# Kernel tuning notes

Hardware: AMD Instinct MI355X
Metric: run time of the kernel (lower is better)

Reference implementation:

```python
import jax, jax.numpy as jnp
import numpy as np
from jax import lax

B, P, ENC = 64, 196, 2048
E, H, A, V = 512, 512, 512, 10000
L = 21  # caption length -> T = 20 decode steps


def setup_inputs() -> dict:
    key = jax.random.key(0)
    ks = jax.random.split(key, 20)
    s = 0.02
    inp = {
        "features": jax.random.normal(ks[0], (B, P, ENC), jnp.float32),
        "captions": jax.random.randint(ks[1], (B, L), 0, V),
        # attention
        "W_enc_att": jax.random.normal(ks[2], (ENC, A), jnp.float32) * s,
        "b_enc_att": jnp.zeros((A,), jnp.float32),
        "W_dec_att": jax.random.normal(ks[3], (H, A), jnp.float32) * s,
        "b_dec_att": jnp.zeros((A,), jnp.float32),
        "W_full": jax.random.normal(ks[4], (A, 1), jnp.float32) * s,
        "b_full": jnp.zeros((1,), jnp.float32),
        # embedding (uniform(-0.1, 0.1) as in init_weights)
        "emb": jax.random.uniform(ks[5], (V, E), jnp.float32, -0.1, 0.1),
        # LSTMCell: input = embed + encoder_dim, gate order i,f,g,o
        "W_ih": jax.random.normal(ks[6], (E + ENC, 4 * H), jnp.float32) * s,
        "W_hh": jax.random.normal(ks[7], (H, 4 * H), jnp.float32) * s,
        "b_ih": jnp.zeros((4 * H,), jnp.float32),
        "b_hh": jnp.zeros((4 * H,), jnp.float32),
        # init state projections
        "W_init_h": jax.random.normal(ks[8], (ENC, H), jnp.float32) * s,
        "b_init_h": jnp.zeros((H,), jnp.float32),
        "W_init_c": jax.random.normal(ks[9], (ENC, H), jnp.float32) * s,
        "b_init_c": jnp.zeros((H,), jnp.float32),
        # gating
        "W_fbeta": jax.random.normal(ks[10], (H, ENC), jnp.float32) * s,
        "b_fbeta": jnp.zeros((ENC,), jnp.float32),
        # output fc (uniform(-0.1,0.1), bias 0)
        "W_fc": jax.random.uniform(ks[11], (H, V), jnp.float32, -0.1, 0.1),
        "b_fc": jnp.zeros((V,), jnp.float32),
    }
    return inp


def reference(features, captions, W_enc_att, b_enc_att, W_dec_att, b_dec_att,
              W_full, b_full, emb, W_ih, W_hh, b_ih, b_hh,
              W_init_h, b_init_h, W_init_c, b_init_c,
              W_fbeta, b_fbeta, W_fc, b_fc):
    # init hidden state from mean-pooled encoder features
    mean_enc = features.mean(axis=1)                       # [B, ENC]
    h0 = mean_enc @ W_init_h + b_init_h                    # [B, H]
    c0 = mean_enc @ W_init_c + b_init_c

    # encoder-side attention projection is time-invariant: precompute
    att1 = features @ W_enc_att + b_enc_att                # [B, P, A]

    T = captions.shape[1] - 1                              # decode_lengths = L-1 (equal lengths)
    embs = emb[captions[:, :T]]                            # [B, T, E]
    embs_t = jnp.swapaxes(embs, 0, 1)                      # [T, B, E]

    def step(carry, e_t):
        h, c = carry
        att2 = h @ W_dec_att + b_dec_att                   # [B, A]
        scores = (jax.nn.relu(att1 + att2[:, None, :]) @ W_full)[..., 0] + b_full  # [B, P]
        alpha = jax.nn.softmax(scores, axis=1)
        awe = jnp.einsum('bp,bpe->be', alpha, features)    # [B, ENC]
        gate = jax.nn.sigmoid(h @ W_fbeta + b_fbeta)
        awe = gate * awe
        x = jnp.concatenate([e_t, awe], axis=1)            # [B, E+ENC]
        gates = x @ W_ih + h @ W_hh + b_ih + b_hh          # [B, 4H]
        i, f, g, o = jnp.split(gates, 4, axis=1)
        c_new = jax.nn.sigmoid(f) * c + jax.nn.sigmoid(i) * jnp.tanh(g)
        h_new = jax.nn.sigmoid(o) * jnp.tanh(c_new)
        preds = h_new @ W_fc + b_fc                        # dropout in eval mode = identity
        return (h_new, c_new), preds

    _, preds = lax.scan(step, (h0, c0), embs_t)            # [T, B, V]
    return jnp.swapaxes(preds, 0, 1)                       # [B, T, V]
```

## Files before the change

### kernel.cpp

```cpp
#include <hip/hip_runtime.h>
#include <hip/hip_bf16.h>


#define TB 256

typedef __bf16 bf16x8 __attribute__((ext_vector_type(8)));
typedef float f32x4 __attribute__((ext_vector_type(4)));
typedef unsigned short u16x8 __attribute__((ext_vector_type(8)));
typedef unsigned short u16x4 __attribute__((ext_vector_type(4)));
typedef unsigned short ushort_t;

__device__ __forceinline__ ushort_t f2bf(float x) {
    unsigned u = __builtin_bit_cast(unsigned, x);
    u += 0x7fffu + ((u >> 16) & 1u);
    return (ushort_t)(u >> 16);
}
__device__ __forceinline__ float bf2f(ushort_t b) {
    return __builtin_bit_cast(float, (unsigned)b << 16);
}
__device__ __forceinline__ void store_pack(
    ushort_t* __restrict__ Ph, ushort_t* __restrict__ Pl,
    int KC, int m, int k, float v)
{
    const size_t flat = ((((size_t)(m >> 4) * KC + (k >> 5)) * 64)
                         + ((k & 31) >> 3) * 16 + (m & 15)) * 8 + (k & 7);
    const ushort_t h = f2bf(v);
    Ph[flat] = h;
    Pl[flat] = f2bf(v - bf2f(h));
}

struct PackJobs {
    const float* W[7];
    ushort_t* Bh[7];
    ushort_t* Bl[7];
    int Nsrc[7], ntCount[7], KC[7], ntBase[7];
    int cum[8];
};

__global__ __launch_bounds__(TB) void pack_all(PackJobs J)
{
    const int blk = blockIdx.x;
    int j = 0;
    #pragma unroll
    for (int i = 1; i < 7; ++i) if (blk >= J.cum[i]) j = i;
    const int g = (blk - J.cum[j]) * TB + threadIdx.x;
    const int KC = J.KC[j];
    const int lane = g & 63;
    const int kc = (g >> 6) % KC;
    const int nt = g / (64 * KC);
    if (nt >= J.ntCount[j]) return;
    const int Nsrc = J.Nsrc[j];
    const float* W = J.W[j];
    const int n = nt * 16 + (lane & 15);
    const int kb = kc * 32 + (lane >> 4) * 8;
    u16x8 hv, lv;
    #pragma unroll
    for (int e = 0; e < 8; ++e) {
        const float x = (n < Nsrc) ? W[(size_t)(kb + e) * Nsrc + n] : 0.f;
        const ushort_t h = f2bf(x);
        hv[e] = h;
        lv[e] = f2bf(x - bf2f(h));
    }
    const size_t flat = (((size_t)(J.ntBase[j] + nt) * KC + kc) * 64 + lane) * 8;
    *(u16x8*)&J.Bh[j][flat] = hv;
    *(u16x8*)&J.Bl[j][flat] = lv;
}

template<int MT, int NT, int WR, int WC>
__device__ __forceinline__ void mfma_tile(
    const ushort_t* lds, int wr, int wc, int lane,
    f32x4 acc[MT / WR][NT / WC])
{
    constexpr int MFR = MT / WR, NFR = NT / WC;
    bf16x8 ah[MFR], al[MFR];
    #pragma unroll
    for (int i = 0; i < MFR; ++i) {
        ah[i] = __builtin_bit_cast(bf16x8, *(const u16x8*)&lds[(wr * MFR + i) * 512 + lane * 8]);
        al[i] = __builtin_bit_cast(bf16x8, *(const u16x8*)&lds[(MT + wr * MFR + i) * 512 + lane * 8]);
    }
    #pragma unroll
    for (int j = 0; j < NFR; ++j) {
        const bf16x8 bh = __builtin_bit_cast(bf16x8, *(const u16x8*)&lds[(2 * MT + wc * NFR + j) * 512 + lane * 8]);
        const bf16x8 bl = __builtin_bit_cast(bf16x8, *(const u16x8*)&lds[(2 * MT + NT + wc * NFR + j) * 512 + lane * 8]);
        #pragma unroll
        for (int i = 0; i < MFR; ++i) {
            acc[i][j] = __builtin_amdgcn_mfma_f32_16x16x32_bf16(ah[i], bh, acc[i][j], 0, 0, 0);
            acc[i][j] = __builtin_amdgcn_mfma_f32_16x16x32_bf16(ah[i], bl, acc[i][j], 0, 0, 0);
            acc[i][j] = __builtin_amdgcn_mfma_f32_16x16x32_bf16(al[i], bh, acc[i][j], 0, 0, 0);
        }
    }
}

template<int MT, int NT, int WR, int WC>
__global__ __launch_bounds__(TB) void gemm_mfma(
    const ushort_t* __restrict__ Ah, const ushort_t* __restrict__ Al,
    const ushort_t* __restrict__ Bh, const ushort_t* __restrict__ Bl,
    int KC, int kcPer,
    const float* __restrict__ bias,
    float* __restrict__ C, int ldc, int Ncols, size_t cPartStride)
{
    constexpr int MFR = MT / WR, NFR = NT / WC, CH = 2 * (MT + NT);
    __shared__ __align__(16) ushort_t lds[CH * 512];
    const int tid = threadIdx.x, wid = tid >> 6, lane = tid & 63;
    const int wr = wid / WC, wc = wid % WC;

    const int tot = gridDim.x * gridDim.y;
    const int lin = blockIdx.x + gridDim.x * blockIdx.y;
    const int q = tot >> 3, r = tot & 7;
    const int xcd = lin & 7, jj = lin >> 3;
    const int base = (xcd < r) ? xcd * (q + 1) : r * (q + 1) + (xcd - r) * q;
    const int lin2 = base + jj;
    const int nb = lin2 / gridDim.y;
    const int mb = lin2 % gridDim.y;

    const int kc0 = blockIdx.z * kcPer;

    f32x4 acc[MFR][NFR];
    #pragma unroll
    for (int i = 0; i < MFR; ++i)
        #pragma unroll
        for (int j = 0; j < NFR; ++j)
            acc[i][j] = f32x4{0.f, 0.f, 0.f, 0.f};

    for (int kc = kc0; kc < kc0 + kcPer; ++kc) {
        __syncthreads();
        #pragma unroll
        for (int cc = 0; cc < CH / 4; ++cc) {
            const int c = cc * 4 + wid;
            const ushort_t* src;
            if (c < MT)                src = Ah + ((size_t)(mb * MT + c) * KC + kc) * 512;
            else if (c < 2 * MT)       src = Al + ((size_t)(mb * MT + c - MT) * KC + kc) * 512;
            else if (c < 2 * MT + NT)  src = Bh + ((size_t)(nb * NT + c - 2 * MT) * KC + kc) * 512;
            else                       src = Bl + ((size_t)(nb * NT + c - 2 * MT - NT) * KC + kc) * 512;
            *(u16x8*)&lds[c * 512 + lane * 8] = *(const u16x8*)(src + lane * 8);
        }
        __syncthreads();
        mfma_tile<MT, NT, WR, WC>(lds, wr, wc, lane, acc);
    }

    C += (size_t)blockIdx.z * cPartStride;
    #pragma unroll
    for (int i = 0; i < MFR; ++i)
        #pragma unroll
        for (int j = 0; j < NFR; ++j) {
            const int col = nb * NT * 16 + (wc * NFR + j) * 16 + (lane & 15);
            if (col < Ncols) {
                const float bv = bias ? bias[col] : 0.f;
                const int rbase = mb * MT * 16 + (wr * MFR + i) * 16 + ((lane >> 4) << 2);
                #pragma unroll
                for (int r2 = 0; r2 < 4; ++r2)
                    C[(size_t)(rbase + r2) * ldc + col] = acc[i][j][r2] + bv;
            }
        }
}

__global__ __launch_bounds__(TB) void gemm_att1(
    const float* __restrict__ A,
    const ushort_t* __restrict__ Bh, const ushort_t* __restrict__ Bl,
    const float* __restrict__ bias, float* __restrict__ C)
{
    __shared__ __align__(16) ushort_t lds[24 * 512];
    const int tid = threadIdx.x, wid = tid >> 6, lane = tid & 63;
    const int wr = wid >> 1, wc = wid & 1;

    const int lin = blockIdx.x + (blockIdx.y << 2);
    const int lin2 = (lin & 7) * 98 + (lin >> 3);
    const int nb = lin2 & 3, mb = lin2 >> 2;

    f32x4 acc[2][4];
    #pragma unroll
    for (int i = 0; i < 2; ++i)
        #pragma unroll
        for (int j = 0; j < 4; ++j)
            acc[i][j] = f32x4{0.f, 0.f, 0.f, 0.f};

    for (int kc = 0; kc < 64; ++kc) {
        __syncthreads();
        #pragma unroll
        for (int cc = 0; cc < 4; ++cc) {
            const int c = cc * 4 + wid;
            const ushort_t* src = (c < 8)
                ? Bh + ((size_t)(nb * 8 + c) * 64 + kc) * 512
                : Bl + ((size_t)(nb * 8 + c - 8) * 64 + kc) * 512;
            *(u16x8*)&lds[(8 + c) * 512 + lane * 8] = *(const u16x8*)(src + lane * 8);
        }
        #pragma unroll
        for (int p = 0; p < 2; ++p) {
            const int id = p * 256 + tid;
            const int row = id >> 3, c4 = id & 7;
            const float4 a = *(const float4*)&A[(size_t)(mb * 64 + row) * 2048 + kc * 32 + c4 * 4];
            const float xv[4] = {a.x, a.y, a.z, a.w};
            u16x4 hv, lv;
            #pragma unroll
            for (int qq = 0; qq < 4; ++qq) {
                const ushort_t h = f2bf(xv[qq]);
                hv[qq] = h;
                lv[qq] = f2bf(xv[qq] - bf2f(h));
            }
            const int base = ((c4 >> 1) * 16 + (row & 15)) * 8 + (c4 & 1) * 4;
            const int chunk = row >> 4;
            *(u16x4*)&lds[chunk * 512 + base] = hv;
            *(u16x4*)&lds[(4 + chunk) * 512 + base] = lv;
        }
        __syncthreads();
        mfma_tile<4, 8, 2, 2>(lds, wr, wc, lane, acc);
    }

    #pragma unroll
    for (int i = 0; i < 2; ++i)
        #pragma unroll
        for (int j = 0; j < 4; ++j) {
            const int col = nb * 128 + (wc * 4 + j) * 16 + (lane & 15);
            const float bv = bias[col];
            const int rbase = mb * 64 + (wr * 2 + i) * 16 + ((lane >> 4) << 2);
            #pragma unroll
            for (int r = 0; r < 4; ++r)
                C[(size_t)(rbase + r) * 512 + col] = acc[i][j][r] + bv;
        }
}

__device__ __forceinline__ void gemm_body(
    float (*As)[68], float (*Ws)[68],
    const float* __restrict__ A, int lda,
    const float* __restrict__ W, int ldw,
    float* __restrict__ C, int ldc,
    int nTile, int N, int K)
{
    const int tid = threadIdx.x;
    const int tn = tid & 15;
    const int tm = tid >> 4;
    const int n0 = nTile * 64;

    float acc[4][4] = {{0.f}};

    for (int k0 = 0; k0 < K; k0 += 32) {
        {
            int r  = tid >> 3;
            int cc = (tid & 7) * 4;
            #pragma unroll
            for (int rr = 0; rr < 64; rr += 32) {
                const float4 a = *(const float4*)&A[(size_t)(rr + r) * lda + (k0 + cc)];
                As[cc + 0][rr + r] = a.x;
                As[cc + 1][rr + r] = a.y;
                As[cc + 2][rr + r] = a.z;
                As[cc + 3][rr + r] = a.w;
            }
        }
        {
            int r  = tid >> 4;
            int cc = (tid & 15) * 4;
            #pragma unroll
            for (int rr = 0; rr < 32; rr += 16) {
                const float4 w = *(const float4*)&W[(size_t)(k0 + rr + r) * ldw + (n0 + cc)];
                *(float4*)&Ws[rr + r][cc] = w;
            }
        }
        __syncthreads();
        #pragma unroll
        for (int kk = 0; kk < 32; ++kk) {
            const float4 a = *(const float4*)&As[kk][tm * 4];
            const float4 w = *(const float4*)&Ws[kk][tn * 4];
            const float av[4] = {a.x, a.y, a.z, a.w};
            const float wv[4] = {w.x, w.y, w.z, w.w};
            #pragma unroll
            for (int i = 0; i < 4; ++i)
                #pragma unroll
                for (int j = 0; j < 4; ++j)
                    acc[i][j] = fmaf(av[i], wv[j], acc[i][j]);
        }
        __syncthreads();
    }

    #pragma unroll
    for (int i = 0; i < 4; ++i) {
        const int m = tm * 4 + i;
        #pragma unroll
        for (int j = 0; j < 4; ++j)
            C[(size_t)m * ldc + (n0 + tn * 4 + j)] = acc[i][j];
    }
}

__global__ __launch_bounds__(TB) void gemm_hc(
    const float* __restrict__ mean,
    const float* __restrict__ Wh0, const float* __restrict__ Wc0,
    float* __restrict__ h0p, float* __restrict__ c0p)
{
    __shared__ float As[32][68];
    __shared__ float Ws[32][68];
    const int ks = blockIdx.y & 7;
    const int which = blockIdx.y >> 3;
    const float* W = which ? Wc0 : Wh0;
    float* Cp = which ? c0p : h0p;
    gemm_body(As, Ws,
              mean + (size_t)ks * 256, 2048,
              W + (size_t)ks * 256 * 512, 512,
              Cp + (size_t)ks * 64 * 512, 512,
              blockIdx.x, 512, 256);
}

__global__ __launch_bounds__(TB) void scores_k(
    const float* __restrict__ att1,
    const float* __restrict__ hga_part,
    const float* __restrict__ bd,
    const float* __restrict__ Wfull,
    float* __restrict__ scores)
{
    const int b = blockIdx.x;
    const int tid = threadIdx.x;
    const int wave = tid >> 6;
    const int lane = tid & 63;

    __shared__ float a2[512];
    __shared__ float wf[512];

    for (int i = tid; i < 512; i += TB) {
        float v = bd[i];
        #pragma unroll
        for (int s = 0; s < 4; ++s)
            v += hga_part[(size_t)s * 64 * 4608 + (size_t)b * 4608 + i];
        a2[i] = v;
        wf[i] = Wfull[i];
    }
    __syncthreads();

    const int p = blockIdx.y * 4 + wave;
    const float* row = att1 + ((size_t)b * 196 + p) * 512;
    float s = 0.f;
    #pragma unroll
    for (int c = 0; c < 512; c += 256) {
        const int k = c + lane * 4;
        const float4 v = *(const float4*)&row[k];
        const float4 av = *(const float4*)&a2[k];
        const float4 wv = *(const float4*)&wf[k];
        s = fmaf(fmaxf(v.x + av.x, 0.f), wv.x, s);
        s = fmaf(fmaxf(v.y + av.y, 0.f), wv.y, s);
        s = fmaf(fmaxf(v.z + av.z, 0.f), wv.z, s);
        s = fmaf(fmaxf(v.w + av.w, 0.f), wv.w, s);
    }
    #pragma unroll
    for (int o = 32; o; o >>= 1) s += __shfl_xor(s, o);
    if (lane == 0) scores[b * 196 + p] = s;
}

__global__ __launch_bounds__(TB) void awe_gate(
    const float* __restrict__ scores,
    const float* __restrict__ features,
    const float* __restrict__ hga_part,
    const float* __restrict__ bf,
    ushort_t* __restrict__ gPh, ushort_t* __restrict__ gPl)
{
    const int b = blockIdx.y, chunk = blockIdx.x;
    const int tid = threadIdx.x;
    const int q = tid >> 6, lane = tid & 63;

    __shared__ float al[196];
    __shared__ float redm[4], reds[4];
    __shared__ float smq[4][256];

    const float sv = (tid < 196) ? scores[b * 196 + tid] : -1e30f;
    float m = sv;
    #pragma unroll
    for (int o = 32; o; o >>= 1) m = fmaxf(m, __shfl_xor(m, o));
    if (lane == 0) redm[q] = m;
    __syncthreads();
    m = fmaxf(fmaxf(redm[0], redm[1]), fmaxf(redm[2], redm[3]));

    const float e = (tid < 196) ? expf(sv - m) : 0.f;
    float s = e;
    #pragma unroll
    for (int o = 32; o; o >>= 1) s += __shfl_xor(s, o);
    if (lane == 0) reds[q] = s;
    __syncthreads();
    s = reds[0] + reds[1] + reds[2] + reds[3];

    if (tid < 196) al[tid] = e / s;
    __syncthreads();

    const int col0 = chunk * 256 + lane * 4;
    const float* f = features + (size_t)b * 196 * 2048 + col0;
    f32x4 acc = {0.f, 0.f, 0.f, 0.f};
    const int p0 = q * 49;
    #pragma unroll 7
    for (int pp = 0; pp < 49; ++pp) {
        const float w = al[p0 + pp];
        const float4 v = *(const float4*)&f[(size_t)(p0 + pp) * 2048];
        acc[0] = fmaf(w, v.x, acc[0]);
        acc[1] = fmaf(w, v.y, acc[1]);
        acc[2] = fmaf(w, v.z, acc[2]);
        acc[3] = fmaf(w, v.w, acc[3]);
    }
    *(f32x4*)&smq[q][lane * 4] = acc;
    __syncthreads();

    const int eg = chunk * 256 + tid;
    const float a = smq[0][tid] + smq[1][tid] + smq[2][tid] + smq[3][tid];
    float gp = bf[eg];
    #pragma unroll
    for (int ss = 0; ss < 4; ++ss)
        gp += hga_part[(size_t)ss * 64 * 4608 + (size_t)b * 4608 + 512 + eg];
    const float gate = 1.f / (1.f + expf(-gp));
    store_pack(gPh, gPl, 64, b, eg, gate * a);
}

__global__ __launch_bounds__(TB) void lstm_pw(
    const float* __restrict__ gates_part,
    const float* __restrict__ hga_part,
    const float* __restrict__ eW,
    const float* __restrict__ b_hh,
    int t,
    float* __restrict__ c,
    ushort_t* __restrict__ hPh, ushort_t* __restrict__ hPl,
    ushort_t* __restrict__ sPh, ushort_t* __restrict__ sPl)
{
    const int idx = blockIdx.x * TB + threadIdx.x;
    const int b = idx >> 9;
    const int j = idx & 511;

    float g[4];
    #pragma unroll
    for (int comp = 0; comp < 4; ++comp) {
        const int col = comp * 512 + j;
        float v = b_hh[col] + eW[((size_t)b * 20 + t) * 2048 + col];
        #pragma unroll
        for (int s = 0; s < 8; ++s)
            v += gates_part[(size_t)s * 64 * 2048 + (size_t)b * 2048 + col];
        #pragma unroll
        for (int s = 0; s < 4; ++s)
            v += hga_part[(size_t)s * 64 * 4608 + (size_t)b * 4608 + 2560 + col];
        g[comp] = v;
    }
    const float si = 1.f / (1.f + expf(-g[0]));
    const float sf = 1.f / (1.f + expf(-g[1]));
    const float gg = tanhf(g[2]);
    const float so = 1.f / (1.f + expf(-g[3]));
    const float cn = sf * c[idx] + si * gg;
    c[idx] = cn;
    const float hn = so * tanhf(cn);
    store_pack(hPh, hPl, 16, b, j, hn);
    store_pack(sPh, sPl, 16, b * 20 + t, j, hn);
}

__global__ __launch_bounds__(TB) void mean_feat(
    const float* __restrict__ features, float* __restrict__ mean_enc)
{
    const int b = blockIdx.y;
    const int e = blockIdx.x * TB + threadIdx.x;
    const float* f = features + (size_t)b * 196 * 2048 + e;
    float s = 0.f;
    #pragma unroll 4
    for (int p = 0; p < 196; ++p) s += f[(size_t)p * 2048];
    mean_enc[b * 2048 + e] = s * (1.f / 196.f);
}

__global__ __launch_bounds__(TB) void gather_emb_pack(
    const int* __restrict__ captions,
    const float* __restrict__ emb,
    ushort_t* __restrict__ Ph, ushort_t* __restrict__ Pl)
{
    const int bt = blockIdx.x;
    const int b = bt / 20;
    const int t = bt % 20;
    const int tok = captions[b * 21 + t];
    for (int e = threadIdx.x; e < 512; e += TB)
        store_pack(Ph, Pl, 16, bt, e, emb[(size_t)tok * 512 + e]);
}

__global__ __launch_bounds__(TB) void reduce_hc(
    const float* __restrict__ h0p, const float* __restrict__ c0p,
    const float* __restrict__ bh0, const float* __restrict__ bc0,
    ushort_t* __restrict__ hPh, ushort_t* __restrict__ hPl,
    float* __restrict__ c)
{
    const int idx = blockIdx.x * TB + threadIdx.x;
    const int half = idx >> 15;
    const int i = idx & 32767;
    const int j = i & 511;
    const float* P = half ? c0p : h0p;
    float v = half ? bc0[j] : bh0[j];
    #pragma unroll
    for (int s = 0; s < 8; ++s) v += P[(size_t)s * 64 * 512 + i];
    if (half) c[i] = v;
    else      store_pack(hPh, hPl, 16, i >> 9, j, v);
}

extern "C" void kernel_launch(void* const* d_in, const int* in_sizes, int n_in,
                              void* d_out, int out_size, void* d_ws, size_t ws_size,
                              hipStream_t stream)
{
    const float* features  = (const float*)d_in[0];
    const int*   captions  = (const int*)  d_in[1];
    const float* W_enc_att = (const float*)d_in[2];
    const float* b_enc_att = (const float*)d_in[3];
    const float* W_dec_att = (const float*)d_in[4];
    const float* b_dec_att = (const float*)d_in[5];
    const float* W_full    = (const float*)d_in[6];
    const float* emb       = (const float*)d_in[8];
    const float* W_ih      = (const float*)d_in[9];
    const float* W_hh      = (const float*)d_in[10];
    const float* b_ih      = (const float*)d_in[11];
    const float* b_hh      = (const float*)d_in[12];
    const float* W_init_h  = (const float*)d_in[13];
    const float* b_init_h  = (const float*)d_in[14];
    const float* W_init_c  = (const float*)d_in[15];
    const float* b_init_c  = (const float*)d_in[16];
    const float* W_fbeta   = (const float*)d_in[17];
    const float* b_fbeta   = (const float*)d_in[18];
    const float* W_fc      = (const float*)d_in[19];
    const float* b_fc      = (const float*)d_in[20];
    float* out = (float*)d_out;
    (void)ws_size;

    float* ws = (float*)d_ws;
    size_t off = 0;
    auto alloc  = [&](size_t n) { float* p = ws + off; off += n; return p; };
    auto ualloc = [&](size_t n) { ushort_t* p = (ushort_t*)(ws + off); off += (n + 1) / 2; return p; };

    float* att1   = alloc((size_t)12544 * 512);
    float* eW     = alloc((size_t)64 * 20 * 2048);
    float* mean   = alloc(64 * 2048);
    float* hga    = alloc((size_t)4 * 64 * 4608);
    float* gatesp = alloc((size_t)8 * 64 * 2048);
    float* c      = alloc(64 * 512);
    float* scores = alloc(64 * 196);

    ushort_t* WencH = ualloc((size_t)32 * 64 * 512);
    ushort_t* WencL = ualloc((size_t)32 * 64 * 512);
    ushort_t* WtopH = ualloc((size_t)128 * 16 * 512);
    ushort_t* WtopL = ualloc((size_t)128 * 16 * 512);
    ushort_t* Wih2H = ualloc((size_t)128 * 64 * 512);
    ushort_t* Wih2L = ualloc((size_t)128 * 64 * 512);
    ushort_t* WdfhH = ualloc((size_t)288 * 16 * 512);
    ushort_t* WdfhL = ualloc((size_t)288 * 16 * 512);
    ushort_t* WfcH  = ualloc((size_t)632 * 16 * 512);
    ushort_t* WfcL  = ualloc((size_t)632 * 16 * 512);
    ushort_t* embsH = ualloc((size_t)80 * 16 * 512);
    ushort_t* embsL = ualloc((size_t)80 * 16 * 512);
    ushort_t* hPh   = ualloc((size_t)4 * 16 * 512);
    ushort_t* hPl   = ualloc((size_t)4 * 16 * 512);
    ushort_t* gPh   = ualloc((size_t)4 * 64 * 512);
    ushort_t* gPl   = ualloc((size_t)4 * 64 * 512);
    ushort_t* sPh   = ualloc((size_t)80 * 16 * 512);
    ushort_t* sPl   = ualloc((size_t)80 * 16 * 512);

    float* h0p = hga;
    float* c0p = gatesp;

    PackJobs J;
    J.W[0]=W_enc_att;               J.Bh[0]=WencH; J.Bl[0]=WencL; J.Nsrc[0]=512;   J.ntCount[0]=32;  J.KC[0]=64; J.ntBase[0]=0;
    J.W[1]=W_ih;                    J.Bh[1]=WtopH; J.Bl[1]=WtopL; J.Nsrc[1]=2048;  J.ntCount[1]=128; J.KC[1]=16; J.ntBase[1]=0;
    J.W[2]=W_ih + (size_t)512*2048; J.Bh[2]=Wih2H; J.Bl[2]=Wih2L; J.Nsrc[2]=2048;  J.ntCount[2]=128; J.KC[2]=64; J.ntBase[2]=0;
    J.W[3]=W_dec_att;               J.Bh[3]=WdfhH; J.Bl[3]=WdfhL; J.Nsrc[3]=512;   J.ntCount[3]=32;  J.KC[3]=16; J.ntBase[3]=0;
    J.W[4]=W_fbeta;                 J.Bh[4]=WdfhH; J.Bl[4]=WdfhL; J.Nsrc[4]=2048;  J.ntCount[4]=128; J.KC[4]=16; J.ntBase[4]=32;
    J.W[5]=W_hh;                    J.Bh[5]=WdfhH; J.Bl[5]=WdfhL; J.Nsrc[5]=2048;  J.ntCount[5]=128; J.KC[5]=16; J.ntBase[5]=160;
    J.W[6]=W_fc;                    J.Bh[6]=WfcH;  J.Bl[6]=WfcL;  J.Nsrc[6]=10000; J.ntCount[6]=632; J.KC[6]=16; J.ntBase[6]=0;
    {
        int cum = 0;
        const int blks[7] = {512, 512, 2048, 128, 512, 512, 2528};
        for (int i = 0; i < 7; ++i) { J.cum[i] = cum; cum += blks[i]; }
        J.cum[7] = cum;
        pack_all<<<cum, TB, 0, stream>>>(J);
    }

    gather_emb_pack<<<1280, TB, 0, stream>>>(captions, emb, embsH, embsL);
    mean_feat<<<dim3(8, 64), TB, 0, stream>>>(features, mean);
    gemm_hc<<<dim3(8, 16), TB, 0, stream>>>(mean, W_init_h, W_init_c, h0p, c0p);
    reduce_hc<<<256, TB, 0, stream>>>(h0p, c0p, b_init_h, b_init_c, hPh, hPl, c);
    gemm_att1<<<dim3(4, 196), TB, 0, stream>>>(features, WencH, WencL, b_enc_att, att1);
    gemm_mfma<8, 8, 2, 2><<<dim3(16, 10, 1), TB, 0, stream>>>(
        embsH, embsL, WtopH, WtopL, 16, 16, b_ih, eW, 2048, 2048, 0);

    for (int t = 0; t < 20; ++t) {
        gemm_mfma<4, 8, 2, 2><<<dim3(36, 1, 4), TB, 0, stream>>>(
            hPh, hPl, WdfhH, WdfhL, 16, 4, nullptr, hga, 4608, 4608, (size_t)64 * 4608);
        scores_k<<<dim3(64, 49), TB, 0, stream>>>(att1, hga, b_dec_att, W_full, scores);
        awe_gate<<<dim3(8, 64), TB, 0, stream>>>(scores, features, hga, b_fbeta, gPh, gPl);
        gemm_mfma<4, 8, 2, 2><<<dim3(16, 1, 8), TB, 0, stream>>>(
            gPh, gPl, Wih2H, Wih2L, 64, 8, nullptr, gatesp, 2048, 2048, (size_t)64 * 2048);
        lstm_pw<<<128, TB, 0, stream>>>(gatesp, hga, eW, b_hh, t, c, hPh, hPl, sPh, sPl);
    }

    gemm_mfma<8, 8, 2, 2><<<dim3(79, 10, 1), TB, 0, stream>>>(
        sPh, sPl, WfcH, WfcL, 16, 16, b_fc, out, 10000, 10000, 0);
}
```

Before: 1.186 ms.

## Store features and att1 in bf16 to halve per-step attention memory traffic

Adds a one-time kernel that converts features to bf16 and has gemm_att1 read this single bf16 copy, dropping the low-part split on the A side. att1 is now written as bf16. The per-step scores and awe kernels read bf16 att1 and features instead of fp32, which halves the bytes streamed over 20 steps. The scores and awe kernels are also reshaped (more rows per wave, 512-thread blocks) to fit the new layout. The cost is lower precision in the attention path, since the features lose their bf16 low part and att1 is rounded.

```diff
diff --git a/kernel.cpp b/kernel.cpp
--- a/kernel.cpp
+++ b/kernel.cpp
@@ -66,6 +66,18 @@
     *(u16x8*)&J.Bl[j][flat] = lv;
 }
 
+__global__ __launch_bounds__(TB) void feat2bf(
+    const float* __restrict__ f, ushort_t* __restrict__ fbf)
+{
+    const size_t i8 = ((size_t)blockIdx.x * TB + threadIdx.x) * 8;
+    const float4 a = *(const float4*)&f[i8];
+    const float4 b = *(const float4*)&f[i8 + 4];
+    u16x8 v;
+    v[0] = f2bf(a.x); v[1] = f2bf(a.y); v[2] = f2bf(a.z); v[3] = f2bf(a.w);
+    v[4] = f2bf(b.x); v[5] = f2bf(b.y); v[6] = f2bf(b.z); v[7] = f2bf(b.w);
+    *(u16x8*)&fbf[i8] = v;
+}
+
 template<int MT, int NT, int WR, int WC>
 __device__ __forceinline__ void mfma_tile(
     const ushort_t* lds, int wr, int wc, int lane,
@@ -155,11 +167,11 @@
 }
 
 __global__ __launch_bounds__(TB) void gemm_att1(
-    const float* __restrict__ A,
+    const ushort_t* __restrict__ fbf,
     const ushort_t* __restrict__ Bh, const ushort_t* __restrict__ Bl,
-    const float* __restrict__ bias, float* __restrict__ C)
-{
-    __shared__ __align__(16) ushort_t lds[24 * 512];
+    const float* __restrict__ bias, ushort_t* __restrict__ att1bf)
+{
+    __shared__ __align__(16) ushort_t lds[20 * 512];
     const int tid = threadIdx.x, wid = tid >> 6, lane = tid & 63;
     const int wr = wid >> 1, wc = wid & 1;
 
@@ -173,6 +185,10 @@
         #pragma unroll
         for (int j = 0; j < 4; ++j)
             acc[i][j] = f32x4{0.f, 0.f, 0.f, 0.f};
+
+    const int arow = tid >> 2, akg = tid & 3;
+    const size_t abase = (size_t)(mb * 64 + arow) * 2048 + akg * 8;
+    const int aldst = (arow >> 4) * 512 + (akg * 16 + (arow & 15)) * 8;
 
     for (int kc = 0; kc < 64; ++kc) {
         __syncthreads();
@@ -182,28 +198,25 @@
             const ushort_t* src = (c < 8)
                 ? Bh + ((size_t)(nb * 8 + c) * 64 + kc) * 512
                 : Bl + ((size_t)(nb * 8 + c - 8) * 64 + kc) * 512;
-            *(u16x8*)&lds[(8 + c) * 512 + lane * 8] = *(const u16x8*)(src + lane * 8);
-        }
-        #pragma unroll
-        for (int p = 0; p < 2; ++p) {
-            const int id = p * 256 + tid;
-            const int row = id >> 3, c4 = id & 7;
-            const float4 a = *(const float4*)&A[(size_t)(mb * 64 + row) * 2048 + kc * 32 + c4 * 4];
-            const float xv[4] = {a.x, a.y, a.z, a.w};
-            u16x4 hv, lv;
+            *(u16x8*)&lds[(4 + c) * 512 + lane * 8] = *(const u16x8*)(src + lane * 8);
+        }
+        *(u16x8*)&lds[aldst] = *(const u16x8*)&fbf[abase + (size_t)kc * 32];
+        __syncthreads();
+
+        bf16x8 ah[2];
+        #pragma unroll
+        for (int i = 0; i < 2; ++i)
+            ah[i] = __builtin_bit_cast(bf16x8, *(const u16x8*)&lds[(wr * 2 + i) * 512 + lane * 8]);
+        #pragma unroll
+        for (int j = 0; j < 4; ++j) {
+            const bf16x8 bh = __builtin_bit_cast(bf16x8, *(const u16x8*)&lds[(4 + wc * 4 + j) * 512 + lane * 8]);
+            const bf16x8 bl = __builtin_bit_cast(bf16x8, *(const u16x8*)&lds[(12 + wc * 4 + j) * 512 + lane * 8]);
             #pragma unroll
-            for (int qq = 0; qq < 4; ++qq) {
-                const ushort_t h = f2bf(xv[qq]);
-                hv[qq] = h;
-                lv[qq] = f2bf(xv[qq] - bf2f(h));
+            for (int i = 0; i < 2; ++i) {
+                acc[i][j] = __builtin_amdgcn_mfma_f32_16x16x32_bf16(ah[i], bh, acc[i][j], 0, 0, 0);
+                acc[i][j] = __builtin_amdgcn_mfma_f32_16x16x32_bf16(ah[i], bl, acc[i][j], 0, 0, 0);
             }
-            const int base = ((c4 >> 1) * 16 + (row & 15)) * 8 + (c4 & 1) * 4;
-            const int chunk = row >> 4;
-            *(u16x4*)&lds[chunk * 512 + base] = hv;
-            *(u16x4*)&lds[(4 + chunk) * 512 + base] = lv;
-        }
-        __syncthreads();
-        mfma_tile<4, 8, 2, 2>(lds, wr, wc, lane, acc);
+        }
     }
 
     #pragma unroll
@@ -215,7 +228,7 @@
             const int rbase = mb * 64 + (wr * 2 + i) * 16 + ((lane >> 4) << 2);
             #pragma unroll
             for (int r = 0; r < 4; ++r)
-                C[(size_t)(rbase + r) * 512 + col] = acc[i][j][r] + bv;
+                att1bf[(size_t)(rbase + r) * 512 + col] = f2bf(acc[i][j][r] + bv);
         }
 }
 
@@ -299,7 +312,7 @@
 }
 
 __global__ __launch_bounds__(TB) void scores_k(
-    const float* __restrict__ att1,
+    const ushort_t* __restrict__ att1bf,
     const float* __restrict__ hga_part,
     const float* __restrict__ bd,
     const float* __restrict__ Wfull,
@@ -323,28 +336,29 @@
     }
     __syncthreads();
 
-    const int p = blockIdx.y * 4 + wave;
-    const float* row = att1 + ((size_t)b * 196 + p) * 512;
-    float s = 0.f;
-    #pragma unroll
-    for (int c = 0; c < 512; c += 256) {
-        const int k = c + lane * 4;
-        const float4 v = *(const float4*)&row[k];
-        const float4 av = *(const float4*)&a2[k];
-        const float4 wv = *(const float4*)&wf[k];
-        s = fmaf(fmaxf(v.x + av.x, 0.f), wv.x, s);
-        s = fmaf(fmaxf(v.y + av.y, 0.f), wv.y, s);
-        s = fmaf(fmaxf(v.z + av.z, 0.f), wv.z, s);
-        s = fmaf(fmaxf(v.w + av.w, 0.f), wv.w, s);
-    }
-    #pragma unroll
-    for (int o = 32; o; o >>= 1) s += __shfl_xor(s, o);
-    if (lane == 0) scores[b * 196 + p] = s;
-}
-
-__global__ __launch_bounds__(TB) void awe_gate(
+    const int k0 = lane * 8;
+    float a2r[8], wfr[8];
+    #pragma unroll
+    for (int e = 0; e < 8; ++e) { a2r[e] = a2[k0 + e]; wfr[e] = wf[k0 + e]; }
+
+    const int p0 = blockIdx.y * 28 + wave * 7;
+    #pragma unroll
+    for (int pp = 0; pp < 7; ++pp) {
+        const int p = p0 + pp;
+        const u16x8 v = *(const u16x8*)&att1bf[((size_t)b * 196 + p) * 512 + k0];
+        float s = 0.f;
+        #pragma unroll
+        for (int e = 0; e < 8; ++e)
+            s = fmaf(fmaxf(bf2f(v[e]) + a2r[e], 0.f), wfr[e], s);
+        #pragma unroll
+        for (int o = 32; o; o >>= 1) s += __shfl_xor(s, o);
+        if (lane == 0) scores[b * 196 + p] = s;
+    }
+}
+
+__global__ __launch_bounds__(512) void awe_gate(
     const float* __restrict__ scores,
-    const float* __restrict__ features,
+    const ushort_t* __restrict__ fbf,
     const float* __restrict__ hga_part,
     const float* __restrict__ bf,
     ushort_t* __restrict__ gPh, ushort_t* __restrict__ gPl)
@@ -354,8 +368,8 @@
     const int q = tid >> 6, lane = tid & 63;
 
     __shared__ float al[196];
-    __shared__ float redm[4], reds[4];
-    __shared__ float smq[4][256];
+    __shared__ float redm[8], reds[8];
+    __shared__ float smq[8][512];
 
     const float sv = (tid < 196) ? scores[b * 196 + tid] : -1e30f;
     float m = sv;
@@ -363,7 +377,9 @@
     for (int o = 32; o; o >>= 1) m = fmaxf(m, __shfl_xor(m, o));
     if (lane == 0) redm[q] = m;
     __syncthreads();
-    m = fmaxf(fmaxf(redm[0], redm[1]), fmaxf(redm[2], redm[3]));
+    m = redm[0];
+    #pragma unroll
+    for (int i = 1; i < 8; ++i) m = fmaxf(m, redm[i]);
 
     const float e = (tid < 196) ? expf(sv - m) : 0.f;
     float s = e;
@@ -371,29 +387,33 @@
     for (int o = 32; o; o >>= 1) s += __shfl_xor(s, o);
     if (lane == 0) reds[q] = s;
     __syncthreads();
-    s = reds[0] + reds[1] + reds[2] + reds[3];
+    s = reds[0];
+    #pragma unroll
+    for (int i = 1; i < 8; ++i) s += reds[i];
 
     if (tid < 196) al[tid] = e / s;
     __syncthreads();
 
-    const int col0 = chunk * 256 + lane * 4;
-    const float* f = features + (size_t)b * 196 * 2048 + col0;
-    f32x4 acc = {0.f, 0.f, 0.f, 0.f};
-    const int p0 = q * 49;
-    #pragma unroll 7
-    for (int pp = 0; pp < 49; ++pp) {
+    const int col0 = chunk * 512 + lane * 8;
+    const ushort_t* f = fbf + (size_t)b * 196 * 2048 + col0;
+    float acc[8] = {0.f, 0.f, 0.f, 0.f, 0.f, 0.f, 0.f, 0.f};
+    const int p0 = q * 25;
+    const int pn = (q == 7) ? 21 : 25;
+    for (int pp = 0; pp < pn; ++pp) {
         const float w = al[p0 + pp];
-        const float4 v = *(const float4*)&f[(size_t)(p0 + pp) * 2048];
-        acc[0] = fmaf(w, v.x, acc[0]);
-        acc[1] = fmaf(w, v.y, acc[1]);
-        acc[2] = fmaf(w, v.z, acc[2]);
-        acc[3] = fmaf(w, v.w, acc[3]);
-    }
-    *(f32x4*)&smq[q][lane * 4] = acc;
+        const u16x8 v = *(const u16x8*)&f[(size_t)(p0 + pp) * 2048];
+        #pragma unroll
+        for (int ee = 0; ee < 8; ++ee)
+            acc[ee] = fmaf(w, bf2f(v[ee]), acc[ee]);
+    }
+    *(f32x4*)&smq[q][lane * 8]     = f32x4{acc[0], acc[1], acc[2], acc[3]};
+    *(f32x4*)&smq[q][lane * 8 + 4] = f32x4{acc[4], acc[5], acc[6], acc[7]};
     __syncthreads();
 
-    const int eg = chunk * 256 + tid;
-    const float a = smq[0][tid] + smq[1][tid] + smq[2][tid] + smq[3][tid];
+    const int eg = chunk * 512 + tid;
+    float a = smq[0][tid];
+    #pragma unroll
+    for (int i = 1; i < 8; ++i) a += smq[i][tid];
     float gp = bf[eg];
     #pragma unroll
     for (int ss = 0; ss < 4; ++ss)
@@ -515,7 +535,6 @@
     auto alloc  = [&](size_t n) { float* p = ws + off; off += n; return p; };
     auto ualloc = [&](size_t n) { ushort_t* p = (ushort_t*)(ws + off); off += (n + 1) / 2; return p; };
 
-    float* att1   = alloc((size_t)12544 * 512);
     float* eW     = alloc((size_t)64 * 20 * 2048);
     float* mean   = alloc(64 * 2048);
     float* hga    = alloc((size_t)4 * 64 * 4608);
@@ -523,6 +542,8 @@
     float* c      = alloc(64 * 512);
     float* scores = alloc(64 * 196);
 
+    ushort_t* fbf    = ualloc((size_t)12544 * 2048);
+    ushort_t* att1bf = ualloc((size_t)12544 * 512);
     ushort_t* WencH = ualloc((size_t)32 * 64 * 512);
     ushort_t* WencL = ualloc((size_t)32 * 64 * 512);
     ushort_t* WtopH = ualloc((size_t)128 * 16 * 512);
@@ -561,19 +582,20 @@
         pack_all<<<cum, TB, 0, stream>>>(J);
     }
 
+    feat2bf<<<12544, TB, 0, stream>>>(features, fbf);
     gather_emb_pack<<<1280, TB, 0, stream>>>(captions, emb, embsH, embsL);
     mean_feat<<<dim3(8, 64), TB, 0, stream>>>(features, mean);
     gemm_hc<<<dim3(8, 16), TB, 0, stream>>>(mean, W_init_h, W_init_c, h0p, c0p);
     reduce_hc<<<256, TB, 0, stream>>>(h0p, c0p, b_init_h, b_init_c, hPh, hPl, c);
-    gemm_att1<<<dim3(4, 196), TB, 0, stream>>>(features, WencH, WencL, b_enc_att, att1);
+    gemm_att1<<<dim3(4, 196), TB, 0, stream>>>(fbf, WencH, WencL, b_enc_att, att1bf);
     gemm_mfma<8, 8, 2, 2><<<dim3(16, 10, 1), TB, 0, stream>>>(
         embsH, embsL, WtopH, WtopL, 16, 16, b_ih, eW, 2048, 2048, 0);
 
     for (int t = 0; t < 20; ++t) {
         gemm_mfma<4, 8, 2, 2><<<dim3(36, 1, 4), TB, 0, stream>>>(
             hPh, hPl, WdfhH, WdfhL, 16, 4, nullptr, hga, 4608, 4608, (size_t)64 * 4608);
-        scores_k<<<dim3(64, 49), TB, 0, stream>>>(att1, hga, b_dec_att, W_full, scores);
-        awe_gate<<<dim3(8, 64), TB, 0, stream>>>(scores, features, hga, b_fbeta, gPh, gPl);
+        scores_k<<<dim3(64, 7), TB, 0, stream>>>(att1bf, hga, b_dec_att, W_full, scores);
+        awe_gate<<<dim3(4, 64), 512, 0, stream>>>(scores, fbf, hga, b_fbeta, gPh, gPl);
         gemm_mfma<4, 8, 2, 2><<<dim3(16, 1, 8), TB, 0, stream>>>(
             gPh, gPl, Wih2H, Wih2L, 64, 8, nullptr, gatesp, 2048, 2048, (size_t)64 * 2048);
         lstm_pw<<<128, TB, 0, stream>>>(gatesp, hga, eW, b_hh, t, c, hPh, hPl, sPh, sPl);
```

Result: faster. 1.056 ms (-11.0%).
